# Optimization experiments

Hardware: AMD Instinct MI355X
Metric: run time of the kernel (lower is better)

Reference implementation:

```python
import jax, jax.numpy as jnp
import numpy as np

GRID_SIZE = 5
SPLINE_ORDER = 3
HIDDEN = 128
IN_FT = 768
BATCH = 32768

def make_grid():
    # uniform grid on [-1, 1] extended by spline_order knots on each side
    h = 2.0 / GRID_SIZE
    return (jnp.arange(-SPLINE_ORDER, GRID_SIZE + SPLINE_ORDER + 1, dtype=jnp.float32) * h - 1.0)

def b_splines(x, grid):
    # x: (B, in) -> bases: (B, in, GRID_SIZE + SPLINE_ORDER) via Cox-de-Boor recursion
    xe = x[..., None]                                  # (B, in, 1)
    bases = ((xe >= grid[:-1]) & (xe < grid[1:])).astype(x.dtype)
    for k in range(1, SPLINE_ORDER + 1):
        left = (xe - grid[:-(k + 1)]) / (grid[k:-1] - grid[:-(k + 1)]) * bases[..., :-1]
        right = (grid[k + 1:] - xe) / (grid[k + 1:] - grid[1:-k]) * bases[..., 1:]
        bases = left + right
    return bases

def kan_layer(x, base_w, spline_w, grid):
    # base_w: (out, in); spline_w: (out, in, G+k)
    B = x.shape[0]
    base_out = jax.nn.silu(x) @ base_w.T
    bas = b_splines(x, grid).reshape(B, -1)            # (B, in*(G+k))
    spline_out = bas @ spline_w.reshape(spline_w.shape[0], -1).T
    return base_out + spline_out

def setup_inputs() -> dict:
    key = jax.random.key(0)
    ks = jax.random.split(key, 8)
    nb = GRID_SIZE + SPLINE_ORDER  # 8 basis functions per edge
    return {
        "stm": jax.random.uniform(ks[0], (BATCH, IN_FT), dtype=jnp.float32),
        "nstm": jax.random.uniform(ks[1], (BATCH, IN_FT), dtype=jnp.float32),
        "ft_w": jax.random.normal(ks[2], (HIDDEN, IN_FT), dtype=jnp.float32) * 0.02,
        "ft_b": jnp.zeros((HIDDEN,), dtype=jnp.float32),
        "kan1_base_w": jax.random.normal(ks[3], (HIDDEN, 2 * HIDDEN), dtype=jnp.float32) * 0.05,
        "kan1_spline_w": jax.random.normal(ks[4], (HIDDEN, 2 * HIDDEN, nb), dtype=jnp.float32) * 0.05,
        "kan2_base_w": jax.random.normal(ks[5], (1, HIDDEN), dtype=jnp.float32) * 0.05,
        "kan2_spline_w": jax.random.normal(ks[6], (1, HIDDEN, nb), dtype=jnp.float32) * 0.05,
    }

def reference(stm, nstm, ft_w, ft_b, kan1_base_w, kan1_spline_w, kan2_base_w, kan2_spline_w):
    grid = make_grid()
    stm_h = stm @ ft_w.T + ft_b
    nstm_h = nstm @ ft_w.T + ft_b
    hidden = jnp.concatenate([stm_h, nstm_h], axis=1)   # (B, 2*HIDDEN)
    hidden = kan_layer(hidden, kan1_base_w, kan1_spline_w, grid)
    out = kan_layer(hidden, kan2_base_w, kan2_spline_w, grid)
    return jax.nn.sigmoid(out)
```

## Files before the change

### kernel.cpp

```cpp
#include <hip/hip_runtime.h>
#include <hip/hip_bf16.h>
#include <math.h>
#include <stdint.h>

typedef __attribute__((ext_vector_type(8))) short bf16x8;
typedef __attribute__((ext_vector_type(4))) float f32x4;

__device__ __forceinline__ uint32_t pack2(float a, float b) {
    union { __hip_bfloat162 h2; uint32_t u; } c;
    c.h2 = __float22bfloat162_rn(make_float2(a, b));
    return c.u;
}
__device__ __forceinline__ unsigned short f2bf(float f) {
    union { __hip_bfloat16 h; unsigned short u; } c;
    c.h = __float2bfloat16(f);
    return c.u;
}
__device__ __forceinline__ float bf2f(unsigned short h) {
    union { uint32_t u; float f; } c; c.u = ((uint32_t)h) << 16;
    return c.f;
}
__device__ __forceinline__ float silu_f(float x) {
    return x / (1.0f + __expf(-x));
}

__device__ __forceinline__ void bspline8(float x, float* __restrict__ b) {
    const float tt = (x + 2.2f) * 2.5f;
#pragma unroll
    for (int v = 0; v < 8; ++v) {
        float y = fabsf(tt - (float)(v + 2));
        float p = fmaxf(2.0f - y, 0.0f);
        float q = fmaxf(1.0f - y, 0.0f);
        b[v] = (p * p * p - 4.0f * q * q * q) * (1.0f / 6.0f);
    }
}

__device__ __forceinline__ void gload16(const void* g, void* l) {
    __builtin_amdgcn_global_load_lds(
        (const __attribute__((address_space(1))) void*)g,
        (__attribute__((address_space(3))) void*)l, 16, 0, 0);
}

__global__ __launch_bounds__(256) void prep_ftw(const float* __restrict__ ftw,
                                                unsigned short* __restrict__ Wb) {
    const int idx = blockIdx.x * 256 + threadIdx.x;
    Wb[idx] = f2bf(ftw[idx]);
}

__global__ __launch_bounds__(256) void prep_bpf(const float* __restrict__ bw,
                                                const float* __restrict__ sw,
                                                unsigned short* __restrict__ BpF) {
    const int idx = blockIdx.x * 256 + threadIdx.x;
    const int e = idx & 7, l = (idx >> 3) & 63, ks = (idx >> 9) & 3;
    const int nt = (idx >> 11) & 1, wc = (idx >> 12) & 3, jb = idx >> 14;
    const int col = wc * 32 + nt * 16 + (l & 15);
    const int k = jb * 128 + ks * 32 + (l >> 4) * 8 + e;
    const int f = k >> 4, v = k & 15;
    float val = 0.f;
    if (v == 0) val = bw[col * 256 + f];
    else if (v <= 8) val = sw[(size_t)(col * 256 + f) * 8 + (v - 1)];
    BpF[idx] = f2bf(val);
}

__global__ __launch_bounds__(512, 4) void kan_fused(
        const float* __restrict__ stm, const float* __restrict__ nstm,
        const unsigned short* __restrict__ Wb, const float* __restrict__ bias,
        const unsigned short* __restrict__ BpF,
        const float* __restrict__ w2b, const float* __restrict__ w2s,
        float* __restrict__ out) {
    __shared__ alignas(16) char lds[81920];
    char* smA  = lds;
    char* smB  = lds + 16384;
    char* smHT = lds + 49152;

    const int r0 = blockIdx.x * 64;
    const int t = threadIdx.x;
    const int l = t & 63, w = t >> 6;
    const int fr = l & 15, h = l >> 4;
    const int wr = w >> 2, wc = w & 3;

    const int arow = t >> 3;
    const int acol = (t & 7) * 16;
    const uint32_t adst0 = (uint32_t)arow * 256u +
        ((uint32_t)(((t & 7) * 2) ^ (arow & 15)) << 4);
    const uint32_t adst1 = (uint32_t)arow * 256u +
        ((uint32_t)(((t & 7) * 2 + 1) ^ (arow & 15)) << 4);
    const int gidx = w * 4;

    f32x4 acc[2][2];
#pragma unroll
    for (int mt = 0; mt < 2; ++mt)
#pragma unroll
        for (int nt = 0; nt < 2; ++nt) acc[mt][nt] = (f32x4){0.f, 0.f, 0.f, 0.f};

    float4 regY[4], regZ[4];
    bf16x8 bf[2][4];

#define FT_ISSUE(REG, TK)                                                      \
    {                                                                          \
        const float* __restrict__ Ap = ((TK) >= 6) ? nstm : stm;               \
        const int kk = ((TK) % 6) * 128;                                       \
        _Pragma("unroll") for (int q = 0; q < 4; ++q)                          \
            REG[q] = *reinterpret_cast<const float4*>(                         \
                &Ap[(size_t)(r0 + arow) * 768 + kk + acol + q * 4]);           \
    }

#define FT_WRITE(REG)                                                          \
    {                                                                          \
        int4 w0, w1;                                                           \
        w0.x = (int)pack2(REG[0].x, REG[0].y);                                 \
        w0.y = (int)pack2(REG[0].z, REG[0].w);                                 \
        w0.z = (int)pack2(REG[1].x, REG[1].y);                                 \
        w0.w = (int)pack2(REG[1].z, REG[1].w);                                 \
        w1.x = (int)pack2(REG[2].x, REG[2].y);                                 \
        w1.y = (int)pack2(REG[2].z, REG[2].w);                                 \
        w1.z = (int)pack2(REG[3].x, REG[3].y);                                 \
        w1.w = (int)pack2(REG[3].z, REG[3].w);                                 \
        *reinterpret_cast<int4*>(smA + adst0) = w0;                            \
        *reinterpret_cast<int4*>(smA + adst1) = w1;                            \
    }

#define GLOADB_FT(K0)                                                          \
    _Pragma("unroll") for (int j = 0; j < 4; ++j) {                            \
        const int col = (gidx + j) * 4 + (l >> 4);                             \
        gload16(&Wb[(size_t)col * 768 + (K0) + (((l & 15) ^ (col & 15)) << 3)],\
                smB + (gidx + j) * 1024);                                      \
    }

#define LOADF(JB)                                                              \
    {                                                                          \
        const unsigned short* __restrict__ fb =                                \
            BpF + (size_t)(JB) * 16384 + wc * 4096 + l * 8;                    \
        _Pragma("unroll") for (int nt = 0; nt < 2; ++nt)                       \
            _Pragma("unroll") for (int ks = 0; ks < 4; ++ks)                   \
                bf[nt][ks] = *reinterpret_cast<const bf16x8*>(                 \
                    fb + nt * 2048 + ks * 512);                                \
    }

#define GEMM_STEP_LDS()                                                        \
    _Pragma("unroll") for (int ks = 0; ks < 4; ++ks) {                         \
        bf16x8 a[2], b[2];                                                     \
        _Pragma("unroll") for (int mt = 0; mt < 2; ++mt) {                     \
            const uint32_t row = (uint32_t)(wr * 32 + mt * 16 + fr);           \
            a[mt] = *reinterpret_cast<const bf16x8*>(                          \
                smA + row * 256u +                                             \
                (((uint32_t)(ks * 4 + h) ^ (row & 15u)) << 4));                \
        }                                                                      \
        _Pragma("unroll") for (int nt = 0; nt < 2; ++nt) {                     \
            const uint32_t col = (uint32_t)(wc * 32 + nt * 16 + fr);           \
            b[nt] = *reinterpret_cast<const bf16x8*>(                          \
                smB + col * 256u +                                             \
                (((uint32_t)(ks * 4 + h) ^ (col & 15u)) << 4));                \
        }                                                                      \
        _Pragma("unroll") for (int mt = 0; mt < 2; ++mt)                       \
            _Pragma("unroll") for (int nt = 0; nt < 2; ++nt)                   \
                acc[mt][nt] = __builtin_amdgcn_mfma_f32_16x16x32_bf16(         \
                    a[mt], b[nt], acc[mt][nt], 0, 0, 0);                       \
    }

#define GEMM_STEP_REG()                                                        \
    _Pragma("unroll") for (int ks = 0; ks < 4; ++ks) {                         \
        bf16x8 a[2];                                                           \
        _Pragma("unroll") for (int mt = 0; mt < 2; ++mt) {                     \
            const uint32_t row = (uint32_t)(wr * 32 + mt * 16 + fr);           \
            a[mt] = *reinterpret_cast<const bf16x8*>(                          \
                smA + row * 256u +                                             \
                (((uint32_t)(ks * 4 + h) ^ (row & 15u)) << 4));                \
        }                                                                      \
        _Pragma("unroll") for (int mt = 0; mt < 2; ++mt)                       \
            _Pragma("unroll") for (int nt = 0; nt < 2; ++nt)                   \
                acc[mt][nt] = __builtin_amdgcn_mfma_f32_16x16x32_bf16(         \
                    a[mt], bf[nt][ks], acc[mt][nt], 0, 0, 0);                  \
    }

#define DUMP_H(SO)                                                             \
    _Pragma("unroll") for (int nt = 0; nt < 2; ++nt) {                         \
        const int col = wc * 32 + nt * 16 + fr;                                \
        const float bv = bias[col];                                            \
        const int feat = (SO) + col;                                           \
        _Pragma("unroll") for (int mt = 0; mt < 2; ++mt) {                     \
            const int rowb = wr * 32 + mt * 16 + h * 4;                        \
            int2 o;                                                            \
            o.x = (int)pack2(acc[mt][nt][0] + bv, acc[mt][nt][1] + bv);        \
            o.y = (int)pack2(acc[mt][nt][2] + bv, acc[mt][nt][3] + bv);        \
            const uint32_t db = (uint32_t)feat * 128u +                        \
                ((uint32_t)((rowb >> 3) ^ (feat & 7)) << 4) +                  \
                (uint32_t)(rowb & 7) * 2u;                                     \
            *reinterpret_cast<int2*>(smHT + db) = o;                           \
            acc[mt][nt] = (f32x4){0.f, 0.f, 0.f, 0.f};                         \
        }                                                                      \
    }

#define LGKM_BAR()                                                             \
    asm volatile("s_waitcnt lgkmcnt(0)" ::: "memory");                         \
    __builtin_amdgcn_sched_barrier(0);                                         \
    __builtin_amdgcn_s_barrier();

    FT_ISSUE(regY, 0);
    FT_ISSUE(regZ, 1);
#pragma unroll 1
    for (int pp = 0; pp < 6; ++pp) {
        FT_WRITE(regY);
        GLOADB_FT(((2 * pp) % 6) * 128);
        __builtin_amdgcn_sched_barrier(0);
        if (pp < 5) {
            FT_ISSUE(regY, 2 * pp + 2);
            asm volatile("s_waitcnt vmcnt(4)" ::: "memory");
        } else {
            asm volatile("s_waitcnt vmcnt(0)" ::: "memory");
        }
        asm volatile("s_waitcnt lgkmcnt(0)" ::: "memory");
        __builtin_amdgcn_sched_barrier(0);
        __builtin_amdgcn_s_barrier();
        __builtin_amdgcn_s_setprio(1);
        GEMM_STEP_LDS();
        __builtin_amdgcn_s_setprio(0);
        LGKM_BAR();
        FT_WRITE(regZ);
        GLOADB_FT(((2 * pp + 1) % 6) * 128);
        __builtin_amdgcn_sched_barrier(0);
        if (pp < 5) {
            FT_ISSUE(regZ, 2 * pp + 3);
            asm volatile("s_waitcnt vmcnt(4)" ::: "memory");
        } else {
            asm volatile("s_waitcnt vmcnt(0)" ::: "memory");
        }
        asm volatile("s_waitcnt lgkmcnt(0)" ::: "memory");
        __builtin_amdgcn_sched_barrier(0);
        __builtin_amdgcn_s_barrier();
        __builtin_amdgcn_s_setprio(1);
        GEMM_STEP_LDS();
        __builtin_amdgcn_s_setprio(0);
        if (pp == 2) { DUMP_H(0); }
        if (pp == 5) { DUMP_H(128); }
        LGKM_BAR();
    }

#pragma unroll 1
    for (int jb = 0; jb < 32; ++jb) {
        LOADF(jb);
        __builtin_amdgcn_sched_barrier(0);
        {
            const int feat = jb * 8 + w;
            const unsigned short xv = *reinterpret_cast<const unsigned short*>(
                smHT + (uint32_t)feat * 128u +
                ((uint32_t)((l >> 3) ^ (feat & 7)) << 4) + (uint32_t)(l & 7) * 2u);
            const float x = bf2f(xv);
            float bs[8];
            bspline8(x, bs);
            const uint32_t pw0 = pack2(silu_f(x), bs[0]);
            const uint32_t pw1 = pack2(bs[1], bs[2]);
            const uint32_t pw2 = pack2(bs[3], bs[4]);
            const uint32_t pw3 = pack2(bs[5], bs[6]);
            const uint32_t pw4 = pack2(bs[7], 0.f);
            const uint32_t d0 = (uint32_t)l * 256u +
                ((uint32_t)((2 * w) ^ (l & 15)) << 4);
            const uint32_t d1 = (uint32_t)l * 256u +
                ((uint32_t)((2 * w + 1) ^ (l & 15)) << 4);
            *reinterpret_cast<int4*>(smA + d0) =
                make_int4((int)pw0, (int)pw1, (int)pw2, (int)pw3);
            *reinterpret_cast<int4*>(smA + d1) = make_int4((int)pw4, 0, 0, 0);
        }
        asm volatile("s_waitcnt lgkmcnt(0)" ::: "memory");
        __builtin_amdgcn_sched_barrier(0);
        __builtin_amdgcn_s_barrier();
        __builtin_amdgcn_s_setprio(1);
        GEMM_STEP_REG();
        __builtin_amdgcn_s_setprio(0);
        LGKM_BAR();
    }

    unsigned short* smH2 = (unsigned short*)lds;
#pragma unroll
    for (int mt = 0; mt < 2; ++mt)
#pragma unroll
        for (int nt = 0; nt < 2; ++nt) {
            const int col = wc * 32 + nt * 16 + fr;
#pragma unroll
            for (int j = 0; j < 4; ++j) {
                const int row = wr * 32 + mt * 16 + h * 4 + j;
                smH2[row * 136 + col] = f2bf(acc[mt][nt][j]);
            }
        }
    __syncthreads();
    const int row2 = t >> 3, qd = t & 7;
    float sum = 0.f;
#pragma unroll 4
    for (int i = 0; i < 16; ++i) {
        const int j = qd * 16 + ((i + qd * 2) & 15);
        const float x = bf2f(smH2[row2 * 136 + j]);
        float bs[8];
        bspline8(x, bs);
        const float4 s0 = *reinterpret_cast<const float4*>(&w2s[j * 8]);
        const float4 s1 = *reinterpret_cast<const float4*>(&w2s[j * 8 + 4]);
        float s = silu_f(x) * w2b[j];
        s += bs[0] * s0.x + bs[1] * s0.y + bs[2] * s0.z + bs[3] * s0.w;
        s += bs[4] * s1.x + bs[5] * s1.y + bs[6] * s1.z + bs[7] * s1.w;
        sum += s;
    }
    sum += __shfl_xor(sum, 1, 64);
    sum += __shfl_xor(sum, 2, 64);
    sum += __shfl_xor(sum, 4, 64);
    if (qd == 0) out[r0 + row2] = 1.0f / (1.0f + __expf(-sum));
}

extern "C" void kernel_launch(void* const* d_in, const int* in_sizes, int n_in,
                              void* d_out, int out_size, void* d_ws, size_t ws_size,
                              hipStream_t stream) {
    const float* stm  = (const float*)d_in[0];
    const float* nstm = (const float*)d_in[1];
    const float* ft_w = (const float*)d_in[2];
    const float* ft_b = (const float*)d_in[3];
    const float* k1bw = (const float*)d_in[4];
    const float* k1sw = (const float*)d_in[5];
    const float* k2bw = (const float*)d_in[6];
    const float* k2sw = (const float*)d_in[7];
    float* out = (float*)d_out;

    char* ws = (char*)d_ws;
    unsigned short* Wb  = (unsigned short*)ws;
    unsigned short* BpF = (unsigned short*)(ws + 196608);

    prep_ftw<<<384, 256, 0, stream>>>(ft_w, Wb);
    prep_bpf<<<2048, 256, 0, stream>>>(k1bw, k1sw, BpF);
    kan_fused<<<512, 512, 0, stream>>>(stm, nstm, Wb, ft_b, BpF, k2bw, k2sw, out);
}
```

Measured before the change: 104.3 us.

## Split KAN layer-1 GEMM into dense spline and deferred SiLU base parts

The layer-1 K dimension was padded to 16 per feature (1 SiLU, 8 bases, 7 zeros), which wasted half the MFMA work and weight bandwidth. Spline bases now form a dense K=8 per feature GEMM. SiLU values are stored in a separate LDS buffer and multiplied by a separately packed base-weight matrix in two tail steps after the loop. This adds a new weight layout, an extra prep kernel and LDS reuse of the smB region, and the base GEMM runs unpipelined at the end.

```diff
diff --git a/kernel.cpp b/kernel.cpp
--- a/kernel.cpp
+++ b/kernel.cpp
@@ -47,30 +47,37 @@
     Wb[idx] = f2bf(ftw[idx]);
 }
 
-__global__ __launch_bounds__(256) void prep_bpf(const float* __restrict__ bw,
-                                                const float* __restrict__ sw,
-                                                unsigned short* __restrict__ BpF) {
+__global__ __launch_bounds__(256) void prep_bwf(const float* __restrict__ bw,
+                                                unsigned short* __restrict__ BwF) {
     const int idx = blockIdx.x * 256 + threadIdx.x;
-    const int e = idx & 7, l = (idx >> 3) & 63, ks = (idx >> 9) & 3;
-    const int nt = (idx >> 11) & 1, wc = (idx >> 12) & 3, jb = idx >> 14;
+    const int e = idx & 7, l = (idx >> 3) & 63, ks = (idx >> 9) & 7;
+    const int nt = (idx >> 12) & 1, wc = (idx >> 13) & 3;
     const int col = wc * 32 + nt * 16 + (l & 15);
-    const int k = jb * 128 + ks * 32 + (l >> 4) * 8 + e;
-    const int f = k >> 4, v = k & 15;
-    float val = 0.f;
-    if (v == 0) val = bw[col * 256 + f];
-    else if (v <= 8) val = sw[(size_t)(col * 256 + f) * 8 + (v - 1)];
-    BpF[idx] = f2bf(val);
+    const int k = ks * 32 + (l >> 4) * 8 + e;
+    BwF[idx] = f2bf(bw[col * 256 + k]);
+}
+
+__global__ __launch_bounds__(256) void prep_swf(const float* __restrict__ sw,
+                                                unsigned short* __restrict__ SwF) {
+    const int idx = blockIdx.x * 256 + threadIdx.x;
+    const int e = idx & 7, l = (idx >> 3) & 63, ks = (idx >> 9) & 1;
+    const int nt = (idx >> 10) & 1, wc = (idx >> 11) & 3, jb = idx >> 13;
+    const int col = wc * 32 + nt * 16 + (l & 15);
+    const int f = jb * 8 + ks * 4 + (l >> 4);
+    SwF[idx] = f2bf(sw[(size_t)(col * 256 + f) * 8 + e]);
 }
 
 __global__ __launch_bounds__(512, 4) void kan_fused(
         const float* __restrict__ stm, const float* __restrict__ nstm,
         const unsigned short* __restrict__ Wb, const float* __restrict__ bias,
-        const unsigned short* __restrict__ BpF,
+        const unsigned short* __restrict__ BwF,
+        const unsigned short* __restrict__ SwF,
         const float* __restrict__ w2b, const float* __restrict__ w2s,
         float* __restrict__ out) {
     __shared__ alignas(16) char lds[81920];
     char* smA  = lds;
     char* smB  = lds + 16384;
+    char* phiS = lds + 16384;
     char* smHT = lds + 49152;
 
     const int r0 = blockIdx.x * 64;
@@ -94,7 +101,8 @@
         for (int nt = 0; nt < 2; ++nt) acc[mt][nt] = (f32x4){0.f, 0.f, 0.f, 0.f};
 
     float4 regY[4], regZ[4];
-    bf16x8 bf[2][4];
+    bf16x8 bsp[2][2];
+    bf16x8 bbw[2][4];
 
 #define FT_ISSUE(REG, TK)                                                      \
     {                                                                          \
@@ -127,14 +135,24 @@
                 smB + (gidx + j) * 1024);                                      \
     }
 
-#define LOADF(JB)                                                              \
+#define LOADSP(JB)                                                             \
     {                                                                          \
         const unsigned short* __restrict__ fb =                                \
-            BpF + (size_t)(JB) * 16384 + wc * 4096 + l * 8;                    \
+            SwF + (size_t)(JB) * 8192 + wc * 2048 + l * 8;                     \
+        _Pragma("unroll") for (int nt = 0; nt < 2; ++nt)                       \
+            _Pragma("unroll") for (int ks = 0; ks < 2; ++ks)                   \
+                bsp[nt][ks] = *reinterpret_cast<const bf16x8*>(                \
+                    fb + nt * 1024 + ks * 512);                                \
+    }
+
+#define LOADBW(HALF)                                                           \
+    {                                                                          \
+        const unsigned short* __restrict__ fb =                                \
+            BwF + wc * 8192 + (HALF) * 2048 + l * 8;                           \
         _Pragma("unroll") for (int nt = 0; nt < 2; ++nt)                       \
             _Pragma("unroll") for (int ks = 0; ks < 4; ++ks)                   \
-                bf[nt][ks] = *reinterpret_cast<const bf16x8*>(                 \
-                    fb + nt * 2048 + ks * 512);                                \
+                bbw[nt][ks] = *reinterpret_cast<const bf16x8*>(                \
+                    fb + nt * 4096 + ks * 512);                                \
     }
 
 #define GEMM_STEP_LDS()                                                        \
@@ -158,19 +176,34 @@
                     a[mt], b[nt], acc[mt][nt], 0, 0, 0);                       \
     }
 
-#define GEMM_STEP_REG()                                                        \
+#define GEMM_SP()                                                              \
+    _Pragma("unroll") for (int ks = 0; ks < 2; ++ks) {                         \
+        bf16x8 a[2];                                                           \
+        _Pragma("unroll") for (int mt = 0; mt < 2; ++mt) {                     \
+            const uint32_t row = (uint32_t)(wr * 32 + mt * 16 + fr);           \
+            a[mt] = *reinterpret_cast<const bf16x8*>(                          \
+                smA + row * 128u +                                             \
+                (((uint32_t)(ks * 4 + h) ^ (row & 7u)) << 4));                 \
+        }                                                                      \
+        _Pragma("unroll") for (int mt = 0; mt < 2; ++mt)                       \
+            _Pragma("unroll") for (int nt = 0; nt < 2; ++nt)                   \
+                acc[mt][nt] = __builtin_amdgcn_mfma_f32_16x16x32_bf16(         \
+                    a[mt], bsp[nt][ks], acc[mt][nt], 0, 0, 0);                 \
+    }
+
+#define GEMM_BW(HALF)                                                          \
     _Pragma("unroll") for (int ks = 0; ks < 4; ++ks) {                         \
         bf16x8 a[2];                                                           \
         _Pragma("unroll") for (int mt = 0; mt < 2; ++mt) {                     \
             const uint32_t row = (uint32_t)(wr * 32 + mt * 16 + fr);           \
             a[mt] = *reinterpret_cast<const bf16x8*>(                          \
-                smA + row * 256u +                                             \
-                (((uint32_t)(ks * 4 + h) ^ (row & 15u)) << 4));                \
+                phiS + row * 512u +                                            \
+                (((uint32_t)(((HALF) * 4 + ks) * 4 + h) ^ (row & 15u)) << 4)); \
         }                                                                      \
         _Pragma("unroll") for (int mt = 0; mt < 2; ++mt)                       \
             _Pragma("unroll") for (int nt = 0; nt < 2; ++nt)                   \
                 acc[mt][nt] = __builtin_amdgcn_mfma_f32_16x16x32_bf16(         \
-                    a[mt], bf[nt][ks], acc[mt][nt], 0, 0, 0);                  \
+                    a[mt], bbw[nt][ks], acc[mt][nt], 0, 0, 0);                 \
     }
 
 #define DUMP_H(SO)                                                             \
@@ -238,7 +271,7 @@
 
 #pragma unroll 1
     for (int jb = 0; jb < 32; ++jb) {
-        LOADF(jb);
+        LOADSP(jb);
         __builtin_amdgcn_sched_barrier(0);
         {
             const int feat = jb * 8 + w;
@@ -248,27 +281,36 @@
             const float x = bf2f(xv);
             float bs[8];
             bspline8(x, bs);
-            const uint32_t pw0 = pack2(silu_f(x), bs[0]);
-            const uint32_t pw1 = pack2(bs[1], bs[2]);
-            const uint32_t pw2 = pack2(bs[3], bs[4]);
-            const uint32_t pw3 = pack2(bs[5], bs[6]);
-            const uint32_t pw4 = pack2(bs[7], 0.f);
-            const uint32_t d0 = (uint32_t)l * 256u +
-                ((uint32_t)((2 * w) ^ (l & 15)) << 4);
-            const uint32_t d1 = (uint32_t)l * 256u +
-                ((uint32_t)((2 * w + 1) ^ (l & 15)) << 4);
-            *reinterpret_cast<int4*>(smA + d0) =
+            const uint32_t pw0 = pack2(bs[0], bs[1]);
+            const uint32_t pw1 = pack2(bs[2], bs[3]);
+            const uint32_t pw2 = pack2(bs[4], bs[5]);
+            const uint32_t pw3 = pack2(bs[6], bs[7]);
+            const uint32_t db = (uint32_t)l * 128u +
+                ((uint32_t)(w ^ (l & 7)) << 4);
+            *reinterpret_cast<int4*>(smA + db) =
                 make_int4((int)pw0, (int)pw1, (int)pw2, (int)pw3);
-            *reinterpret_cast<int4*>(smA + d1) = make_int4((int)pw4, 0, 0, 0);
+            const uint32_t ds = (uint32_t)l * 512u +
+                ((uint32_t)(jb ^ (l & 15)) << 4) + (uint32_t)w * 2u;
+            *reinterpret_cast<unsigned short*>(phiS + ds) = f2bf(silu_f(x));
         }
         asm volatile("s_waitcnt lgkmcnt(0)" ::: "memory");
         __builtin_amdgcn_sched_barrier(0);
         __builtin_amdgcn_s_barrier();
         __builtin_amdgcn_s_setprio(1);
-        GEMM_STEP_REG();
+        GEMM_SP();
         __builtin_amdgcn_s_setprio(0);
         LGKM_BAR();
     }
+
+    LOADBW(0);
+    __builtin_amdgcn_s_setprio(1);
+    GEMM_BW(0);
+    __builtin_amdgcn_s_setprio(0);
+    LOADBW(1);
+    __builtin_amdgcn_s_setprio(1);
+    GEMM_BW(1);
+    __builtin_amdgcn_s_setprio(0);
+    LGKM_BAR();
 
     unsigned short* smH2 = (unsigned short*)lds;
 #pragma unroll
@@ -319,9 +361,12 @@
 
     char* ws = (char*)d_ws;
     unsigned short* Wb  = (unsigned short*)ws;
-    unsigned short* BpF = (unsigned short*)(ws + 196608);
+    unsigned short* BwF = (unsigned short*)(ws + 196608);
+    unsigned short* SwF = (unsigned short*)(ws + 262144);
 
     prep_ftw<<<384, 256, 0, stream>>>(ft_w, Wb);
-    prep_bpf<<<2048, 256, 0, stream>>>(k1bw, k1sw, BpF);
-    kan_fused<<<512, 512, 0, stream>>>(stm, nstm, Wb, ft_b, BpF, k2bw, k2sw, out);
-}
+    prep_bwf<<<128, 256, 0, stream>>>(k1bw, BwF);
+    prep_swf<<<1024, 256, 0, stream>>>(k1sw, SwF);
+    kan_fused<<<512, 512, 0, stream>>>(stm, nstm, Wb, ft_b, BwF, SwF,
+                                       k2bw, k2sw, out);
+}
```

Result: faster. 93.04 us, median of 2 (-10.8%).
